# Kernel tuning notes

Measured on AMD Instinct MI355X. Metric: run time of the kernel, lower is better.

Reference implementation:

```python
import jax, jax.numpy as jnp
import numpy as np

N_NODES = 50000
N_EDGES = 160000
D = 512
N_GRAPHS = 64
EPS = 1e-5


def setup_inputs() -> dict:
    key = jax.random.key(0)
    ks = jax.random.split(key, 8)
    node = jax.random.normal(ks[0], (N_NODES, D), dtype=jnp.float32)
    edge_index = jax.random.randint(ks[1], (2, N_EDGES), 0, N_NODES, dtype=jnp.int64)
    edge_attr = jax.random.uniform(ks[2], (N_EDGES,), dtype=jnp.float32)
    batch_ptr = jnp.sort(jax.random.randint(ks[3], (N_NODES,), 0, N_GRAPHS, dtype=jnp.int64))
    W = jax.random.normal(ks[4], (D, D), dtype=jnp.float32) / np.float32(np.sqrt(D))
    b = jnp.zeros((D,), dtype=jnp.float32)
    gn_weight = jnp.ones((D,), dtype=jnp.float32)
    gn_bias = jnp.zeros((D,), dtype=jnp.float32)
    gn_mean_scale = jnp.ones((D,), dtype=jnp.float32)
    return {"node": node, "edge_attr": edge_attr, "W": W, "b": b,
            "gn_weight": gn_weight, "gn_bias": gn_bias, "gn_mean_scale": gn_mean_scale,
            "edge_index": edge_index, "batch_ptr": batch_ptr}


def _gcn_conv(x, edge_index, edge_weight, W, b):
    # x: [N, D]. PyG GCNConv(normalize=True): lin -> add self-loops -> D^-1/2 A D^-1/2 -> + bias
    x = x @ W  # [N, D]
    loop = jnp.arange(N_NODES, dtype=edge_index.dtype)
    row = jnp.concatenate([edge_index[0], loop])  # source
    col = jnp.concatenate([edge_index[1], loop])  # target
    w = jnp.concatenate([edge_weight, jnp.ones((N_NODES,), dtype=x.dtype)])
    deg = jax.ops.segment_sum(w, col, num_segments=N_NODES)  # weighted in-degree incl. self-loop
    dis = jnp.where(deg > 0, jax.lax.rsqrt(deg), 0.0)
    norm = dis[row] * w * dis[col]  # [E+N]
    msgs = x[row] * norm[:, None]  # gather + scale
    out = jax.ops.segment_sum(msgs, col, num_segments=N_NODES)  # scatter-add
    return out + b


def _graph_norm(x, batch, weight, bias, mean_scale):
    # PyG GraphNorm: per-graph mean/var over nodes, learnable mean scale alpha
    ones = jnp.ones((x.shape[0],), dtype=x.dtype)
    count = jax.ops.segment_sum(ones, batch, num_segments=N_GRAPHS)  # [G]
    count = jnp.maximum(count, 1.0)[:, None]
    mean = jax.ops.segment_sum(x, batch, num_segments=N_GRAPHS) / count  # [G, D]
    centered = x - mean[batch] * mean_scale  # [N, D]
    var = jax.ops.segment_sum(centered * centered, batch, num_segments=N_GRAPHS) / count
    inv_std = jax.lax.rsqrt(var + EPS)  # [G, D]
    return weight * centered * inv_std[batch] + bias


def reference(node, edge_attr, W, b, gn_weight, gn_bias, gn_mean_scale, edge_index, batch_ptr):
    conv = _gcn_conv(node, edge_index, edge_attr, W, b)
    h = node + conv  # skip_connection=True
    h = _graph_norm(h, batch_ptr, gn_weight, gn_bias, gn_mean_scale)
    return jax.nn.relu(h)
```

## Files before the change

kernel.cpp:

```cpp
#include <hip/hip_runtime.h>


#define N_NODES 50000
#define PADN    50048
#define N_EDGES 160000
#define DIM 512
#define N_GRAPHS 64
#define EPSV 1e-5f
#define NBLK 196

typedef short short8 __attribute__((ext_vector_type(8)));
typedef float floatx4 __attribute__((ext_vector_type(4)));

__device__ __forceinline__ unsigned short f2bf(float x) {
    unsigned int u = __float_as_uint(x);
    u += 0x7FFFu + ((u >> 16) & 1u);
    return (unsigned short)(u >> 16);
}
__device__ __forceinline__ float bf2f(unsigned short s) {
    return __uint_as_float(((unsigned int)s) << 16);
}

__global__ __launch_bounds__(256) void k_init(float* __restrict__ deg,
                                              float* __restrict__ Sx,
                                              float* __restrict__ Sxx,
                                              float* __restrict__ cntg,
                                              int* __restrict__ ecnt) {
    int i = blockIdx.x * 256 + threadIdx.x;
    if (i < N_NODES) { deg[i] = 1.0f; ecnt[i] = 0; }
    if (i < N_GRAPHS * DIM) { Sx[i] = 0.f; Sxx[i] = 0.f; }
    if (i < N_GRAPHS) cntg[i] = 0.f;
}

__global__ __launch_bounds__(256) void k_deg(const int* __restrict__ ei,
                                             const float* __restrict__ ew,
                                             float* __restrict__ deg,
                                             int* __restrict__ ecnt) {
    int e = blockIdx.x * 256 + threadIdx.x;
    if (e < N_EDGES) {
        int c = ei[N_EDGES + e];
        atomicAdd(&deg[c], ew[e]);
        atomicAdd(&ecnt[c], 1);
    }
}

__global__ __launch_bounds__(256) void k_scanA(const int* __restrict__ ecnt,
                                               int* __restrict__ bsum) {
    int i = blockIdx.x * 256 + threadIdx.x;
    int v = (i < N_NODES) ? ecnt[i] : 0;
#pragma unroll
    for (int off = 32; off; off >>= 1) v += __shfl_down(v, off, 64);
    __shared__ int ws[4];
    if ((threadIdx.x & 63) == 0) ws[threadIdx.x >> 6] = v;
    __syncthreads();
    if (threadIdx.x == 0) bsum[blockIdx.x] = ws[0] + ws[1] + ws[2] + ws[3];
}

__global__ __launch_bounds__(256) void k_scanB(const int* __restrict__ bsum,
                                               int* __restrict__ bbase) {
    __shared__ int s[256];
    int t = threadIdx.x;
    int v = (t < NBLK) ? bsum[t] : 0;
    s[t] = v;
    __syncthreads();
#pragma unroll
    for (int off = 1; off < 256; off <<= 1) {
        int u = (t >= off) ? s[t - off] : 0;
        __syncthreads();
        s[t] += u;
        __syncthreads();
    }
    if (t <= NBLK) bbase[t] = (t == 0) ? 0 : s[t - 1];
}

__global__ __launch_bounds__(256) void k_scanC(const int* __restrict__ ecnt,
                                               const int* __restrict__ bbase,
                                               int* __restrict__ rowptr,
                                               int* __restrict__ cursor,
                                               float* __restrict__ deg) {
    __shared__ int s[256];
    int t = threadIdx.x;
    int i = blockIdx.x * 256 + t;
    int v = (i < N_NODES) ? ecnt[i] : 0;
    s[t] = v;
    __syncthreads();
#pragma unroll
    for (int off = 1; off < 256; off <<= 1) {
        int u = (t >= off) ? s[t - off] : 0;
        __syncthreads();
        s[t] += u;
        __syncthreads();
    }
    int excl = s[t] - v + bbase[blockIdx.x];
    if (i <= N_NODES) rowptr[i] = excl;
    if (i < N_NODES) {
        cursor[i] = excl;
        deg[i] = rsqrtf(deg[i]);
    }
}

__global__ __launch_bounds__(256) void k_fill(const int* __restrict__ ei,
                                              const float* __restrict__ ew,
                                              const float* __restrict__ dis,
                                              int* __restrict__ cursor,
                                              int* __restrict__ srcs,
                                              float* __restrict__ wts) {
    int e = blockIdx.x * 256 + threadIdx.x;
    if (e >= N_EDGES) return;
    int r = ei[e];
    int c = ei[N_EDGES + e];
    int pos = atomicAdd(&cursor[c], 1);
    srcs[pos] = r;
    wts[pos] = ew[e] * dis[r];
}

__global__ __launch_bounds__(256) void k_cast(const float* __restrict__ node,
                                              short* __restrict__ nodeB) {
    size_t idx = (size_t)blockIdx.x * 256 + threadIdx.x;
    size_t base = idx * 8;
    int row = (int)(base >> 9);
    int4 o;
    if (row >= N_NODES) {
        o = make_int4(0, 0, 0, 0);
    } else {
        float4 a = *(const float4*)&node[base];
        float4 c = *(const float4*)&node[base + 4];
        o.x = ((unsigned)f2bf(a.y) << 16) | f2bf(a.x);
        o.y = ((unsigned)f2bf(a.w) << 16) | f2bf(a.z);
        o.z = ((unsigned)f2bf(c.y) << 16) | f2bf(c.x);
        o.w = ((unsigned)f2bf(c.w) << 16) | f2bf(c.z);
    }
    *(int4*)&nodeB[base] = o;
}

__global__ __launch_bounds__(256) void k_prep_w(const float* __restrict__ W,
                                                short* __restrict__ Wt) {
    int i = blockIdx.x * 256 + threadIdx.x;
    int k = i >> 9, n = i & 511;
    Wt[n * 512 + k] = (short)f2bf(W[i]);
}

__global__ __launch_bounds__(256) void k_gemm_mfma(const short* __restrict__ Abf,
                                                   const short* __restrict__ Bt,
                                                   short* __restrict__ Cbf) {
    __shared__ short As[128 * 64];
    __shared__ short Bs[128 * 64];
    const int tid  = threadIdx.x;
    const int wave = tid >> 6;
    const int lane = tid & 63;
    const int l16  = lane & 15;
    const int quad = lane >> 4;
    const int row0 = blockIdx.y * 128;
    const int col0 = blockIdx.x * 128;
    const int mb = (wave >> 1) * 64;
    const int nb = (wave & 1) * 64;

    floatx4 acc[4][4];
    const floatx4 z = {0.f, 0.f, 0.f, 0.f};
#pragma unroll
    for (int i = 0; i < 4; ++i)
#pragma unroll
        for (int j = 0; j < 4; ++j) acc[i][j] = z;

    const int srow = lane >> 3;
    const int scol = (lane & 7) * 8;

    for (int kk = 0; kk < DIM; kk += 64) {
#pragma unroll
        for (int j = 0; j < 4; ++j) {
            int seg = wave * 4 + j;
            int r = seg * 8 + srow;
            __builtin_amdgcn_global_load_lds(
                (const __attribute__((address_space(1))) void*)(Abf + (size_t)(row0 + r) * DIM + kk + scol),
                (__attribute__((address_space(3))) void*)(As + seg * 512 + lane * 8),
                16, 0, 0);
            __builtin_amdgcn_global_load_lds(
                (const __attribute__((address_space(1))) void*)(Bt + (size_t)(col0 + r) * DIM + kk + scol),
                (__attribute__((address_space(3))) void*)(Bs + seg * 512 + lane * 8),
                16, 0, 0);
        }
        __syncthreads();
#pragma unroll
        for (int kh = 0; kh < 2; ++kh) {
            short8 af[4], bfr[4];
#pragma unroll
            for (int i = 0; i < 4; ++i)
                af[i] = *(const short8*)&As[(mb + i * 16 + l16) * 64 + kh * 32 + quad * 8];
#pragma unroll
            for (int j = 0; j < 4; ++j)
                bfr[j] = *(const short8*)&Bs[(nb + j * 16 + l16) * 64 + kh * 32 + quad * 8];
#pragma unroll
            for (int i = 0; i < 4; ++i)
#pragma unroll
                for (int j = 0; j < 4; ++j)
                    acc[i][j] = __builtin_amdgcn_mfma_f32_16x16x32_bf16(af[i], bfr[j], acc[i][j], 0, 0, 0);
        }
        __syncthreads();
    }
#pragma unroll
    for (int i = 0; i < 4; ++i)
#pragma unroll
        for (int j = 0; j < 4; ++j) {
            int col = col0 + nb + j * 16 + l16;
#pragma unroll
            for (int r = 0; r < 4; ++r) {
                int row = row0 + mb + i * 16 + quad * 4 + r;
                Cbf[(size_t)row * DIM + col] = (short)f2bf(acc[i][j][r]);
            }
        }
}

__global__ __launch_bounds__(256) void k_gather_stats(
        const int* __restrict__ rowptr,
        const int* __restrict__ srcs,
        const float* __restrict__ wts,
        const short* __restrict__ xWb,
        short* __restrict__ nodeB,
        const float* __restrict__ b,
        const float* __restrict__ dis,
        const int* __restrict__ batch,
        float* __restrict__ Sx,
        float* __restrict__ Sxx,
        float* __restrict__ cntg) {
    const int half = threadIdx.x >> 7;
    const int q = (threadIdx.x & 127) * 4;
    const int lead = (threadIdx.x & 127) == 0;
    const int n0 = blockIdx.x * 32;
    float4 bb = *(const float4*)&b[q];
    float sx0 = 0.f, sx1 = 0.f, sx2 = 0.f, sx3 = 0.f;
    float xx0 = 0.f, xx1 = 0.f, xx2 = 0.f, xx3 = 0.f;
    int cur = -1, cnt = 0;
    for (int r = 0; r < 16; ++r) {
        int n = n0 + r * 2 + half;
        if (n >= N_NODES) break;
        int g = batch[n];
        if (g != cur) {
            if (cur >= 0) {
                atomicAdd(&Sx[cur * DIM + q + 0], sx0);
                atomicAdd(&Sx[cur * DIM + q + 1], sx1);
                atomicAdd(&Sx[cur * DIM + q + 2], sx2);
                atomicAdd(&Sx[cur * DIM + q + 3], sx3);
                atomicAdd(&Sxx[cur * DIM + q + 0], xx0);
                atomicAdd(&Sxx[cur * DIM + q + 1], xx1);
                atomicAdd(&Sxx[cur * DIM + q + 2], xx2);
                atomicAdd(&Sxx[cur * DIM + q + 3], xx3);
                if (lead) atomicAdd(&cntg[cur], (float)cnt);
                sx0 = sx1 = sx2 = sx3 = 0.f;
                xx0 = xx1 = xx2 = xx3 = 0.f;
                cnt = 0;
            }
            cur = g;
        }
        float dn = dis[n];
        int lo = rowptr[n], hi = rowptr[n + 1];
        ushort4 xs = *(const ushort4*)&xWb[(size_t)n * DIM + q];
        float a0 = dn * bf2f(xs.x), a1 = dn * bf2f(xs.y);
        float a2 = dn * bf2f(xs.z), a3 = dn * bf2f(xs.w);
        for (int i = lo; i < hi; ++i) {
            int s = srcs[i];
            float w = wts[i];
            ushort4 v = *(const ushort4*)&xWb[(size_t)s * DIM + q];
            a0 += w * bf2f(v.x); a1 += w * bf2f(v.y);
            a2 += w * bf2f(v.z); a3 += w * bf2f(v.w);
        }
        ushort4 nv = *(const ushort4*)&nodeB[(size_t)n * DIM + q];
        float h0 = bf2f(nv.x) + bb.x + dn * a0;
        float h1 = bf2f(nv.y) + bb.y + dn * a1;
        float h2 = bf2f(nv.z) + bb.z + dn * a2;
        float h3 = bf2f(nv.w) + bb.w + dn * a3;
        sx0 += h0; xx0 += h0 * h0;
        sx1 += h1; xx1 += h1 * h1;
        sx2 += h2; xx2 += h2 * h2;
        sx3 += h3; xx3 += h3 * h3;
        cnt++;
        ushort4 hv;
        hv.x = f2bf(h0); hv.y = f2bf(h1); hv.z = f2bf(h2); hv.w = f2bf(h3);
        *(ushort4*)&nodeB[(size_t)n * DIM + q] = hv;
    }
    if (cur >= 0) {
        atomicAdd(&Sx[cur * DIM + q + 0], sx0);
        atomicAdd(&Sx[cur * DIM + q + 1], sx1);
        atomicAdd(&Sx[cur * DIM + q + 2], sx2);
        atomicAdd(&Sx[cur * DIM + q + 3], sx3);
        atomicAdd(&Sxx[cur * DIM + q + 0], xx0);
        atomicAdd(&Sxx[cur * DIM + q + 1], xx1);
        atomicAdd(&Sxx[cur * DIM + q + 2], xx2);
        atomicAdd(&Sxx[cur * DIM + q + 3], xx3);
        if (lead) atomicAdd(&cntg[cur], (float)cnt);
    }
}

__global__ __launch_bounds__(256) void k_fin(const float* __restrict__ Sx,
                                             const float* __restrict__ Sxx,
                                             const float* __restrict__ cntg,
                                             const float* __restrict__ alpha,
                                             float* __restrict__ mA,
                                             float* __restrict__ inv) {
    int i = blockIdx.x * 256 + threadIdx.x;
    if (i >= N_GRAPHS * DIM) return;
    int d = i & (DIM - 1);
    int g = i >> 9;
    float c = fmaxf(cntg[g], 1.0f);
    float m = Sx[i] / c;
    float ma = m * alpha[d];
    float var = Sxx[i] / c - 2.f * m * ma + ma * ma;
    mA[i] = ma;
    inv[i] = rsqrtf(var + EPSV);
}

__global__ __launch_bounds__(256) void k_norm(const short* __restrict__ hB,
                                              const int* __restrict__ batch,
                                              const float* __restrict__ mA,
                                              const float* __restrict__ inv,
                                              const float* __restrict__ gw,
                                              const float* __restrict__ gb,
                                              float* __restrict__ out) {
    size_t idx = (size_t)blockIdx.x * 256 + threadIdx.x;
    int n = (int)(idx >> 7);
    int q = ((int)idx & 127) * 4;
    if (n >= N_NODES) return;
    int g = batch[n];
    ushort4 hv = *(const ushort4*)&hB[(size_t)n * DIM + q];
    float4 ma = *(const float4*)&mA[(size_t)g * DIM + q];
    float4 iv = *(const float4*)&inv[(size_t)g * DIM + q];
    float4 w4 = *(const float4*)&gw[q];
    float4 b4 = *(const float4*)&gb[q];
    float4 r;
    r.x = fmaxf(0.f, (bf2f(hv.x) - ma.x) * iv.x * w4.x + b4.x);
    r.y = fmaxf(0.f, (bf2f(hv.y) - ma.y) * iv.y * w4.y + b4.y);
    r.z = fmaxf(0.f, (bf2f(hv.z) - ma.z) * iv.z * w4.z + b4.z);
    r.w = fmaxf(0.f, (bf2f(hv.w) - ma.w) * iv.w * w4.w + b4.w);
    *(float4*)&out[(size_t)n * DIM + q] = r;
}

extern "C" void kernel_launch(void* const* d_in, const int* in_sizes, int n_in,
                              void* d_out, int out_size, void* d_ws, size_t ws_size,
                              hipStream_t stream) {
    const float* node  = (const float*)d_in[0];
    const float* eattr = (const float*)d_in[1];
    const float* W     = (const float*)d_in[2];
    const float* b     = (const float*)d_in[3];
    const float* gw    = (const float*)d_in[4];
    const float* gb    = (const float*)d_in[5];
    const float* alpha = (const float*)d_in[6];
    const int*   ei    = (const int*)d_in[7];
    const int*   batch = (const int*)d_in[8];
    float* out = (float*)d_out;

    short* nodeB = (short*)d_ws;
    short* xWb   = nodeB + (size_t)PADN * DIM;
    short* Wt    = xWb + (size_t)PADN * DIM;
    float* dis   = (float*)(Wt + DIM * DIM);
    float* Sx    = dis + N_NODES;
    float* Sxx   = Sx + N_GRAPHS * DIM;
    float* cntg  = Sxx + N_GRAPHS * DIM;
    float* mA    = cntg + 64;
    float* inv   = mA + N_GRAPHS * DIM;
    float* wts   = inv + N_GRAPHS * DIM;
    int* ecnt    = (int*)(wts + N_EDGES);
    int* rowptr  = ecnt + N_NODES;
    int* cursor  = rowptr + N_NODES + 1;
    int* srcs    = cursor + N_NODES;
    int* bsum    = srcs + N_EDGES;
    int* bbase   = bsum + NBLK;

    k_init<<<196, 256, 0, stream>>>(dis, Sx, Sxx, cntg, ecnt);
    k_deg<<<(N_EDGES + 255) / 256, 256, 0, stream>>>(ei, eattr, dis, ecnt);
    k_scanA<<<NBLK, 256, 0, stream>>>(ecnt, bsum);
    k_scanB<<<1, 256, 0, stream>>>(bsum, bbase);
    k_scanC<<<NBLK, 256, 0, stream>>>(ecnt, bbase, rowptr, cursor, dis);
    k_fill<<<(N_EDGES + 255) / 256, 256, 0, stream>>>(ei, eattr, dis, cursor, srcs, wts);
    k_cast<<<(PADN * DIM / 8 + 255) / 256, 256, 0, stream>>>(node, nodeB);
    k_prep_w<<<(DIM * DIM + 255) / 256, 256, 0, stream>>>(W, Wt);
    dim3 ggrid(4, PADN / 128);
    k_gemm_mfma<<<ggrid, 256, 0, stream>>>(nodeB, Wt, xWb);
    k_gather_stats<<<(N_NODES + 31) / 32, 256, 0, stream>>>(rowptr, srcs, wts, xWb,
                                                            nodeB, b, dis, batch,
                                                            Sx, Sxx, cntg);
    k_fin<<<128, 256, 0, stream>>>(Sx, Sxx, cntg, alpha, mA, inv);
    k_norm<<<25000, 256, 0, stream>>>(nodeB, batch, mA, inv, gw, gb, out);
}
```

Before: 416.7 us.

## Merge setup kernels, split gather from stats, fold finalize into norm

Folds the cast, weight transpose and init kernels into a single setup launch, and folds the per-graph finalize step into the norm kernel. The gather is split out into its own kernel with one wave per node and 8 bf16 elements per lane, so neighbour row loads are wider; the per-graph statistics move to a separate pass that rereads the stored h. The aim is fewer launches and better gather efficiency. The cost is an extra read of h, and recomputing rsqrt per element in the norm kernel.

```diff
diff --git a/kernel.cpp b/kernel.cpp
--- a/kernel.cpp
+++ b/kernel.cpp
@@ -20,16 +20,49 @@
 __device__ __forceinline__ float bf2f(unsigned short s) {
     return __uint_as_float(((unsigned int)s) << 16);
 }
-
-__global__ __launch_bounds__(256) void k_init(float* __restrict__ deg,
-                                              float* __restrict__ Sx,
-                                              float* __restrict__ Sxx,
-                                              float* __restrict__ cntg,
-                                              int* __restrict__ ecnt) {
-    int i = blockIdx.x * 256 + threadIdx.x;
-    if (i < N_NODES) { deg[i] = 1.0f; ecnt[i] = 0; }
-    if (i < N_GRAPHS * DIM) { Sx[i] = 0.f; Sxx[i] = 0.f; }
-    if (i < N_GRAPHS) cntg[i] = 0.f;
+__device__ __forceinline__ float bflo(int p) {
+    return __uint_as_float(((unsigned int)p) << 16);
+}
+__device__ __forceinline__ float bfhi(int p) {
+    return __uint_as_float(((unsigned int)p) & 0xFFFF0000u);
+}
+
+__global__ __launch_bounds__(256) void k_setup(const float* __restrict__ node,
+                                               const float* __restrict__ W,
+                                               short* __restrict__ nodeB,
+                                               short* __restrict__ Wt,
+                                               float* __restrict__ deg,
+                                               float* __restrict__ Sx,
+                                               float* __restrict__ Sxx,
+                                               float* __restrict__ cntg,
+                                               int* __restrict__ ecnt) {
+    int t = threadIdx.x;
+    size_t idx = (size_t)blockIdx.x * 256 + t;
+    size_t base = idx * 8;
+    int row = (int)(base >> 9);
+    int4 o;
+    if (row >= N_NODES) {
+        o = make_int4(0, 0, 0, 0);
+    } else {
+        float4 a = *(const float4*)&node[base];
+        float4 c = *(const float4*)&node[base + 4];
+        o.x = ((unsigned)f2bf(a.y) << 16) | f2bf(a.x);
+        o.y = ((unsigned)f2bf(a.w) << 16) | f2bf(a.z);
+        o.z = ((unsigned)f2bf(c.y) << 16) | f2bf(c.x);
+        o.w = ((unsigned)f2bf(c.w) << 16) | f2bf(c.z);
+    }
+    *(int4*)&nodeB[base] = o;
+    if (blockIdx.x < 1024) {
+        int i = blockIdx.x * 256 + t;
+        int k = i >> 9, n = i & 511;
+        Wt[n * 512 + k] = (short)f2bf(W[i]);
+    }
+    if (blockIdx.x < NBLK) {
+        int i = blockIdx.x * 256 + t;
+        if (i < N_NODES) { deg[i] = 1.0f; ecnt[i] = 0; }
+        if (i < N_GRAPHS * DIM) { Sx[i] = 0.f; Sxx[i] = 0.f; }
+        if (i < N_GRAPHS) cntg[i] = 0.f;
+    }
 }
 
 __global__ __launch_bounds__(256) void k_deg(const int* __restrict__ ei,
@@ -112,32 +145,6 @@
     int pos = atomicAdd(&cursor[c], 1);
     srcs[pos] = r;
     wts[pos] = ew[e] * dis[r];
-}
-
-__global__ __launch_bounds__(256) void k_cast(const float* __restrict__ node,
-                                              short* __restrict__ nodeB) {
-    size_t idx = (size_t)blockIdx.x * 256 + threadIdx.x;
-    size_t base = idx * 8;
-    int row = (int)(base >> 9);
-    int4 o;
-    if (row >= N_NODES) {
-        o = make_int4(0, 0, 0, 0);
-    } else {
-        float4 a = *(const float4*)&node[base];
-        float4 c = *(const float4*)&node[base + 4];
-        o.x = ((unsigned)f2bf(a.y) << 16) | f2bf(a.x);
-        o.y = ((unsigned)f2bf(a.w) << 16) | f2bf(a.z);
-        o.z = ((unsigned)f2bf(c.y) << 16) | f2bf(c.x);
-        o.w = ((unsigned)f2bf(c.w) << 16) | f2bf(c.z);
-    }
-    *(int4*)&nodeB[base] = o;
-}
-
-__global__ __launch_bounds__(256) void k_prep_w(const float* __restrict__ W,
-                                                short* __restrict__ Wt) {
-    int i = blockIdx.x * 256 + threadIdx.x;
-    int k = i >> 9, n = i & 511;
-    Wt[n * 512 + k] = (short)f2bf(W[i]);
 }
 
 __global__ __launch_bounds__(256) void k_gemm_mfma(const short* __restrict__ Abf,
@@ -210,23 +217,64 @@
         }
 }
 
-__global__ __launch_bounds__(256) void k_gather_stats(
-        const int* __restrict__ rowptr,
-        const int* __restrict__ srcs,
-        const float* __restrict__ wts,
-        const short* __restrict__ xWb,
-        short* __restrict__ nodeB,
-        const float* __restrict__ b,
-        const float* __restrict__ dis,
-        const int* __restrict__ batch,
-        float* __restrict__ Sx,
-        float* __restrict__ Sxx,
-        float* __restrict__ cntg) {
+__global__ __launch_bounds__(256) void k_gather(const int* __restrict__ rowptr,
+                                                const int* __restrict__ srcs,
+                                                const float* __restrict__ wts,
+                                                const short* __restrict__ xWb,
+                                                short* __restrict__ nodeB,
+                                                const float* __restrict__ b,
+                                                const float* __restrict__ dis) {
+    const int lane = threadIdx.x & 63;
+    const int n = __builtin_amdgcn_readfirstlane(blockIdx.x * 4 + (threadIdx.x >> 6));
+    const int q = lane * 8;
+    const float dn = dis[n];
+    const int lo = rowptr[n], hi = rowptr[n + 1];
+
+    float a0, a1, a2, a3, a4, a5, a6, a7;
+    {
+        int4 raw = *(const int4*)&xWb[(size_t)n * DIM + q];
+        a0 = dn * bflo(raw.x); a1 = dn * bfhi(raw.x);
+        a2 = dn * bflo(raw.y); a3 = dn * bfhi(raw.y);
+        a4 = dn * bflo(raw.z); a5 = dn * bfhi(raw.z);
+        a6 = dn * bflo(raw.w); a7 = dn * bfhi(raw.w);
+    }
+    for (int i = lo; i < hi; ++i) {
+        int s = srcs[i];
+        float w = wts[i];
+        int4 raw = *(const int4*)&xWb[(size_t)s * DIM + q];
+        a0 = fmaf(w, bflo(raw.x), a0); a1 = fmaf(w, bfhi(raw.x), a1);
+        a2 = fmaf(w, bflo(raw.y), a2); a3 = fmaf(w, bfhi(raw.y), a3);
+        a4 = fmaf(w, bflo(raw.z), a4); a5 = fmaf(w, bfhi(raw.z), a5);
+        a6 = fmaf(w, bflo(raw.w), a6); a7 = fmaf(w, bfhi(raw.w), a7);
+    }
+    int4 nd = *(const int4*)&nodeB[(size_t)n * DIM + q];
+    float4 b0 = *(const float4*)&b[q];
+    float4 b1 = *(const float4*)&b[q + 4];
+    float h0 = bflo(nd.x) + b0.x + dn * a0;
+    float h1 = bfhi(nd.x) + b0.y + dn * a1;
+    float h2 = bflo(nd.y) + b0.z + dn * a2;
+    float h3 = bfhi(nd.y) + b0.w + dn * a3;
+    float h4 = bflo(nd.z) + b1.x + dn * a4;
+    float h5 = bfhi(nd.z) + b1.y + dn * a5;
+    float h6 = bflo(nd.w) + b1.z + dn * a6;
+    float h7 = bfhi(nd.w) + b1.w + dn * a7;
+    int4 o;
+    o.x = ((unsigned)f2bf(h1) << 16) | f2bf(h0);
+    o.y = ((unsigned)f2bf(h3) << 16) | f2bf(h2);
+    o.z = ((unsigned)f2bf(h5) << 16) | f2bf(h4);
+    o.w = ((unsigned)f2bf(h7) << 16) | f2bf(h6);
+    *(int4*)&nodeB[(size_t)n * DIM + q] = o;
+}
+
+__global__ __launch_bounds__(256) void k_stats(const short* __restrict__ hB,
+                                               const int* __restrict__ batch,
+                                               float* __restrict__ Sx,
+                                               float* __restrict__ Sxx,
+                                               float* __restrict__ cntg) {
     const int half = threadIdx.x >> 7;
     const int q = (threadIdx.x & 127) * 4;
     const int lead = (threadIdx.x & 127) == 0;
     const int n0 = blockIdx.x * 32;
-    float4 bb = *(const float4*)&b[q];
     float sx0 = 0.f, sx1 = 0.f, sx2 = 0.f, sx3 = 0.f;
     float xx0 = 0.f, xx1 = 0.f, xx2 = 0.f, xx3 = 0.f;
     int cur = -1, cnt = 0;
@@ -251,31 +299,13 @@
             }
             cur = g;
         }
-        float dn = dis[n];
-        int lo = rowptr[n], hi = rowptr[n + 1];
-        ushort4 xs = *(const ushort4*)&xWb[(size_t)n * DIM + q];
-        float a0 = dn * bf2f(xs.x), a1 = dn * bf2f(xs.y);
-        float a2 = dn * bf2f(xs.z), a3 = dn * bf2f(xs.w);
-        for (int i = lo; i < hi; ++i) {
-            int s = srcs[i];
-            float w = wts[i];
-            ushort4 v = *(const ushort4*)&xWb[(size_t)s * DIM + q];
-            a0 += w * bf2f(v.x); a1 += w * bf2f(v.y);
-            a2 += w * bf2f(v.z); a3 += w * bf2f(v.w);
-        }
-        ushort4 nv = *(const ushort4*)&nodeB[(size_t)n * DIM + q];
-        float h0 = bf2f(nv.x) + bb.x + dn * a0;
-        float h1 = bf2f(nv.y) + bb.y + dn * a1;
-        float h2 = bf2f(nv.z) + bb.z + dn * a2;
-        float h3 = bf2f(nv.w) + bb.w + dn * a3;
+        ushort4 hv = *(const ushort4*)&hB[(size_t)n * DIM + q];
+        float h0 = bf2f(hv.x), h1 = bf2f(hv.y), h2 = bf2f(hv.z), h3 = bf2f(hv.w);
         sx0 += h0; xx0 += h0 * h0;
         sx1 += h1; xx1 += h1 * h1;
         sx2 += h2; xx2 += h2 * h2;
         sx3 += h3; xx3 += h3 * h3;
         cnt++;
-        ushort4 hv;
-        hv.x = f2bf(h0); hv.y = f2bf(h1); hv.z = f2bf(h2); hv.w = f2bf(h3);
-        *(ushort4*)&nodeB[(size_t)n * DIM + q] = hv;
     }
     if (cur >= 0) {
         atomicAdd(&Sx[cur * DIM + q + 0], sx0);
@@ -290,28 +320,12 @@
     }
 }
 
-__global__ __launch_bounds__(256) void k_fin(const float* __restrict__ Sx,
-                                             const float* __restrict__ Sxx,
-                                             const float* __restrict__ cntg,
-                                             const float* __restrict__ alpha,
-                                             float* __restrict__ mA,
-                                             float* __restrict__ inv) {
-    int i = blockIdx.x * 256 + threadIdx.x;
-    if (i >= N_GRAPHS * DIM) return;
-    int d = i & (DIM - 1);
-    int g = i >> 9;
-    float c = fmaxf(cntg[g], 1.0f);
-    float m = Sx[i] / c;
-    float ma = m * alpha[d];
-    float var = Sxx[i] / c - 2.f * m * ma + ma * ma;
-    mA[i] = ma;
-    inv[i] = rsqrtf(var + EPSV);
-}
-
 __global__ __launch_bounds__(256) void k_norm(const short* __restrict__ hB,
                                               const int* __restrict__ batch,
-                                              const float* __restrict__ mA,
-                                              const float* __restrict__ inv,
+                                              const float* __restrict__ Sx,
+                                              const float* __restrict__ Sxx,
+                                              const float* __restrict__ cntg,
+                                              const float* __restrict__ alpha,
                                               const float* __restrict__ gw,
                                               const float* __restrict__ gb,
                                               float* __restrict__ out) {
@@ -320,16 +334,25 @@
     int q = ((int)idx & 127) * 4;
     if (n >= N_NODES) return;
     int g = batch[n];
-    ushort4 hv = *(const ushort4*)&hB[(size_t)n * DIM + q];
-    float4 ma = *(const float4*)&mA[(size_t)g * DIM + q];
-    float4 iv = *(const float4*)&inv[(size_t)g * DIM + q];
+    float c = fmaxf(cntg[g], 1.0f);
+    float rc = __builtin_amdgcn_rcpf(c);
+    float4 sx = *(const float4*)&Sx[(size_t)g * DIM + q];
+    float4 xx = *(const float4*)&Sxx[(size_t)g * DIM + q];
+    float4 al = *(const float4*)&alpha[q];
     float4 w4 = *(const float4*)&gw[q];
     float4 b4 = *(const float4*)&gb[q];
+    ushort4 hv = *(const ushort4*)&hB[(size_t)n * DIM + q];
+    float m0 = sx.x * rc, m1 = sx.y * rc, m2 = sx.z * rc, m3 = sx.w * rc;
+    float ma0 = m0 * al.x, ma1 = m1 * al.y, ma2 = m2 * al.z, ma3 = m3 * al.w;
+    float iv0 = rsqrtf(xx.x * rc - 2.f * m0 * ma0 + ma0 * ma0 + EPSV);
+    float iv1 = rsqrtf(xx.y * rc - 2.f * m1 * ma1 + ma1 * ma1 + EPSV);
+    float iv2 = rsqrtf(xx.z * rc - 2.f * m2 * ma2 + ma2 * ma2 + EPSV);
+    float iv3 = rsqrtf(xx.w * rc - 2.f * m3 * ma3 + ma3 * ma3 + EPSV);
     float4 r;
-    r.x = fmaxf(0.f, (bf2f(hv.x) - ma.x) * iv.x * w4.x + b4.x);
-    r.y = fmaxf(0.f, (bf2f(hv.y) - ma.y) * iv.y * w4.y + b4.y);
-    r.z = fmaxf(0.f, (bf2f(hv.z) - ma.z) * iv.z * w4.z + b4.z);
-    r.w = fmaxf(0.f, (bf2f(hv.w) - ma.w) * iv.w * w4.w + b4.w);
+    r.x = fmaxf(0.f, (bf2f(hv.x) - ma0) * iv0 * w4.x + b4.x);
+    r.y = fmaxf(0.f, (bf2f(hv.y) - ma1) * iv1 * w4.y + b4.y);
+    r.z = fmaxf(0.f, (bf2f(hv.z) - ma2) * iv2 * w4.z + b4.z);
+    r.w = fmaxf(0.f, (bf2f(hv.w) - ma3) * iv3 * w4.w + b4.w);
     *(float4*)&out[(size_t)n * DIM + q] = r;
 }
 
@@ -354,9 +377,7 @@
     float* Sx    = dis + N_NODES;
     float* Sxx   = Sx + N_GRAPHS * DIM;
     float* cntg  = Sxx + N_GRAPHS * DIM;
-    float* mA    = cntg + 64;
-    float* inv   = mA + N_GRAPHS * DIM;
-    float* wts   = inv + N_GRAPHS * DIM;
+    float* wts   = cntg + 64;
     int* ecnt    = (int*)(wts + N_EDGES);
     int* rowptr  = ecnt + N_NODES;
     int* cursor  = rowptr + N_NODES + 1;
@@ -364,19 +385,16 @@
     int* bsum    = srcs + N_EDGES;
     int* bbase   = bsum + NBLK;
 
-    k_init<<<196, 256, 0, stream>>>(dis, Sx, Sxx, cntg, ecnt);
+    k_setup<<<PADN * DIM / 8 / 256, 256, 0, stream>>>(node, W, nodeB, Wt,
+                                                      dis, Sx, Sxx, cntg, ecnt);
     k_deg<<<(N_EDGES + 255) / 256, 256, 0, stream>>>(ei, eattr, dis, ecnt);
     k_scanA<<<NBLK, 256, 0, stream>>>(ecnt, bsum);
     k_scanB<<<1, 256, 0, stream>>>(bsum, bbase);
     k_scanC<<<NBLK, 256, 0, stream>>>(ecnt, bbase, rowptr, cursor, dis);
     k_fill<<<(N_EDGES + 255) / 256, 256, 0, stream>>>(ei, eattr, dis, cursor, srcs, wts);
-    k_cast<<<(PADN * DIM / 8 + 255) / 256, 256, 0, stream>>>(node, nodeB);
-    k_prep_w<<<(DIM * DIM + 255) / 256, 256, 0, stream>>>(W, Wt);
     dim3 ggrid(4, PADN / 128);
     k_gemm_mfma<<<ggrid, 256, 0, stream>>>(nodeB, Wt, xWb);
-    k_gather_stats<<<(N_NODES + 31) / 32, 256, 0, stream>>>(rowptr, srcs, wts, xWb,
-                                                            nodeB, b, dis, batch,
-                                                            Sx, Sxx, cntg);
-    k_fin<<<128, 256, 0, stream>>>(Sx, Sxx, cntg, alpha, mA, inv);
-    k_norm<<<25000, 256, 0, stream>>>(nodeB, batch, mA, inv, gw, gb, out);
-}
+    k_gather<<<N_NODES / 4, 256, 0, stream>>>(rowptr, srcs, wts, xWb, nodeB, b, dis);
+    k_stats<<<(N_NODES + 31) / 32, 256, 0, stream>>>(nodeB, batch, Sx, Sxx, cntg);
+    k_norm<<<25000, 256, 0, stream>>>(nodeB, batch, Sx, Sxx, cntg, alpha, gw, gb, out);
+}
```

Measured after the change: 413.2 us. Within noise of the previous version (-0.9%).
